# Optimization experiments

Hardware: AMD Instinct MI355X
Metric: run time of the kernel (lower is better)

The kernel has to match this reference:

```python
import jax, jax.numpy as jnp
import numpy as np

KS = 3          # kernel_size
NH = 6          # num_heads
NUM_TOK = KS ** 3  # 27 neighbors per query


def setup_inputs() -> dict:
    key = jax.random.key(0)
    k1, k2, k3 = jax.random.split(key, 3)
    q = jax.random.normal(k1, (1, 40, 40, 40, 96), dtype=jnp.float32)
    k = jax.random.normal(k2, (1, 40, 40, 40, 96), dtype=jnp.float32)
    rpb = jax.random.normal(k3, (NH, KS, KS, KS), dtype=jnp.float32) * 0.02
    return {"q": q, "k": k, "rpb": rpb}


def _offsets():
    # torch.arange(-3//2+1, 3//2+1) == arange(-1, 2); meshgrid 'ij'; stacked -> [27, 3]
    r = jnp.arange(-1, 2, dtype=jnp.float32)
    g = jnp.stack(jnp.meshgrid(r, r, r, indexing="ij"), axis=-1)
    return g.reshape(NUM_TOK, 3)


def reference(q, k, rpb):
    B, H, W, T, C = q.shape
    hd = C // NH
    scale = hd ** -0.5
    N = H * W * T

    # queries: [B, N, nh, hd], pre-scaled
    qh = q.reshape(B, N, NH, hd) * scale

    # zero-pad keys by 1 voxel on each spatial side (matches nnf.pad on channels-first k)
    kp = jnp.pad(jnp.transpose(k, (0, 4, 1, 2, 3)),
                 ((0, 0), (0, 0), (1, 1), (1, 1), (1, 1)))

    # 27 shifted views == torch unfold over a 3x3x3 window (i slowest, matches grid order)
    wins = [kp[:, :, i:i + H, j:j + W, l:l + T]
            for i in range(KS) for j in range(KS) for l in range(KS)]
    Kw = jnp.stack(wins, axis=2)                 # [B, C, 27, H, W, T]
    Kw = Kw.reshape(B, NH, hd, NUM_TOK, N)        # [B, nh, hd, 27, N]

    # attention logits over the 27-token neighborhood
    attn = jnp.einsum("bnhd,bhdkn->bnhk", qh, Kw)  # [B, N, nh, 27]
    attn = attn + rpb.reshape(NH, NUM_TOK)[None, None, :, :]  # relative position bias
    attn = jax.nn.softmax(attn, axis=-1)

    # expected displacement: weighted sum of integer offsets -> [B, N, nh, 3]
    x = jnp.einsum("bnhk,kc->bnhc", attn, _offsets())
    x = x.reshape(B, H, W, T, NH * 3)
    return jnp.transpose(x, (0, 4, 1, 2, 3))      # [B, nh*3, H, W, T]
```

## Files before the change

kernel.cpp:

```cpp
#include <hip/hip_runtime.h>

typedef _Float16 h2 __attribute__((ext_vector_type(2)));

#define DH 40
#define DW 40
#define DT 40
#define NC 96
#define NH 6
#define HD 16
#define NTOK 27
#define NVOX (DH * DW * DT)

#define TX 8
#define TY 4
#define TZ 8
#define HX 10
#define HY 6
#define HZ 10
#define NHALO (HX * HY * HZ)
#define ROW_I4 3

#define TXN (DH / TX)
#define TYN (DW / TY)
#define TZN (DT / TZ)
#define NTILE (TXN * TYN * TZN)
#define NJOB (NTILE * NH)
#define NXCD 8
#define GRID 1504
#define PER_XCD (GRID / NXCD)

__device__ __forceinline__ float dot2acc(h2 a, h2 b, float c) {
    return __builtin_amdgcn_fdot2(a, b, c, false);
}

__device__ __forceinline__ h2 pkrtz(float a, float b) {
    return __builtin_bit_cast(h2, __builtin_amdgcn_cvt_pkrtz(a, b));
}

union I4H {
    int4 v[2];
    h2 h[8];
};

__global__ __launch_bounds__(256) void natt_disp_kernel(
    const float* __restrict__ q,
    const float* __restrict__ k,
    const float* __restrict__ rpb,
    float* __restrict__ out)
{
    __shared__ int4 s_k[NHALO * ROW_I4];

    const int job = (blockIdx.x & (NXCD - 1)) * PER_XCD + (blockIdx.x >> 3);
    if (job >= NJOB) return;

    const int h    = job % NH;
    const int tile = job / NH;
    const int tz = tile % TZN;
    const int ty = (tile / TZN) % TYN;
    const int tx = tile / (TZN * TYN);
    const int x0 = tx * TX, y0 = ty * TY, z0 = tz * TZ;

    const int tid = threadIdx.x;

    float rk[NTOK];
    {
        const float* rb = rpb + h * NTOK;
        #pragma unroll
        for (int kk = 0; kk < NTOK; ++kk) rk[kk] = rb[kk];
    }

    #pragma unroll
    for (int it = 0; it < 3; ++it) {
        const int n = tid + it * 256;
        if (n < NHALO) {
            const int hx = n / (HY * HZ);
            const int r  = n - hx * (HY * HZ);
            const int hy = r / HZ;
            const int hz = r - hy * HZ;
            const int gx = x0 - 1 + hx;
            const int gy = y0 - 1 + hy;
            const int gz = z0 - 1 + hz;
            I4H u;
            u.v[0] = make_int4(0, 0, 0, 0);
            u.v[1] = make_int4(0, 0, 0, 0);
            if (((unsigned)gx < DH) & ((unsigned)gy < DW) & ((unsigned)gz < DT)) {
                const float* src = k + ((size_t)((gx * DW + gy) * DT + gz)) * NC
                                     + h * HD;
                const float4 a = *(const float4*)(src);
                const float4 b = *(const float4*)(src + 4);
                const float4 c = *(const float4*)(src + 8);
                const float4 d = *(const float4*)(src + 12);
                u.h[0] = pkrtz(a.x, a.y);
                u.h[1] = pkrtz(a.z, a.w);
                u.h[2] = pkrtz(b.x, b.y);
                u.h[3] = pkrtz(b.z, b.w);
                u.h[4] = pkrtz(c.x, c.y);
                u.h[5] = pkrtz(c.z, c.w);
                u.h[6] = pkrtz(d.x, d.y);
                u.h[7] = pkrtz(d.z, d.w);
            }
            s_k[n * ROW_I4 + 0] = u.v[0];
            s_k[n * ROW_I4 + 1] = u.v[1];
        }
    }

    const int lz = tid & (TZ - 1);
    const int ly = (tid >> 3) & (TY - 1);
    const int lx = tid >> 5;
    const int vox = ((x0 + lx) * DW + (y0 + ly)) * DT + (z0 + lz);

    h2 qh[8];
    {
        const float4* qv = (const float4*)(q + (size_t)vox * NC + h * HD);
        const float4 a = qv[0], b = qv[1], c = qv[2], d = qv[3];
        qh[0] = pkrtz(a.x, a.y);
        qh[1] = pkrtz(a.z, a.w);
        qh[2] = pkrtz(b.x, b.y);
        qh[3] = pkrtz(b.z, b.w);
        qh[4] = pkrtz(c.x, c.y);
        qh[5] = pkrtz(c.z, c.w);
        qh[6] = pkrtz(d.x, d.y);
        qh[7] = pkrtz(d.z, d.w);
    }

    __syncthreads();

    float l[NTOK];
    #pragma unroll
    for (int i = 0; i < 3; ++i) {
        #pragma unroll
        for (int j = 0; j < 3; ++j) {
            const int base = ((lx + i) * HY + (ly + j)) * HZ + lz;
            #pragma unroll
            for (int ll = 0; ll < 3; ++ll) {
                const int n = base + ll;
                I4H u;
                u.v[0] = s_k[n * ROW_I4 + 0];
                u.v[1] = s_k[n * ROW_I4 + 1];
                float d = 0.0f;
                d = dot2acc(qh[0], u.h[0], d);
                d = dot2acc(qh[1], u.h[1], d);
                d = dot2acc(qh[2], u.h[2], d);
                d = dot2acc(qh[3], u.h[3], d);
                d = dot2acc(qh[4], u.h[4], d);
                d = dot2acc(qh[5], u.h[5], d);
                d = dot2acc(qh[6], u.h[6], d);
                d = dot2acc(qh[7], u.h[7], d);
                const int kk = (i * 3 + j) * 3 + ll;
                l[kk] = fmaf(d, 0.25f, rk[kk]);
            }
        }
    }

    float g0 = fmaxf(fmaxf(l[0],  l[1]),  l[2]);
    float g1 = fmaxf(fmaxf(l[3],  l[4]),  l[5]);
    float g2 = fmaxf(fmaxf(l[6],  l[7]),  l[8]);
    float g3 = fmaxf(fmaxf(l[9],  l[10]), l[11]);
    float g4 = fmaxf(fmaxf(l[12], l[13]), l[14]);
    float g5 = fmaxf(fmaxf(l[15], l[16]), l[17]);
    float g6 = fmaxf(fmaxf(l[18], l[19]), l[20]);
    float g7 = fmaxf(fmaxf(l[21], l[22]), l[23]);
    float g8 = fmaxf(fmaxf(l[24], l[25]), l[26]);
    float t0 = fmaxf(fmaxf(g0, g1), g2);
    float t1 = fmaxf(fmaxf(g3, g4), g5);
    float t2 = fmaxf(fmaxf(g6, g7), g8);
    const float m = fmaxf(fmaxf(t0, t1), t2);

    const float LOG2E = 1.44269504f;
    const float nm2 = -m * LOG2E;
    float e[NTOK];
    #pragma unroll
    for (int kk = 0; kk < NTOK; ++kk)
        e[kk] = exp2f(fmaf(l[kk], LOG2E, nm2));

    float s[9], zp[9];
    #pragma unroll
    for (int g = 0; g < 9; ++g) {
        s[g]  = (e[g * 3] + e[g * 3 + 1]) + e[g * 3 + 2];
        zp[g] = e[g * 3 + 2] - e[g * 3];
    }
    const float sum = ((s[0] + s[1]) + (s[2] + s[3]))
                    + ((s[4] + s[5]) + (s[6] + s[7])) + s[8];
    const float szs = ((zp[0] + zp[1]) + (zp[2] + zp[3]))
                    + ((zp[4] + zp[5]) + (zp[6] + zp[7])) + zp[8];
    const float sxs = ((s[6] + s[7]) + s[8]) - ((s[0] + s[1]) + s[2]);
    const float sys = ((s[2] + s[5]) + s[8]) - ((s[0] + s[3]) + s[6]);

    const float inv = __builtin_amdgcn_rcpf(sum);

    out[((size_t)(h * 3 + 0)) * NVOX + vox] = sxs * inv;
    out[((size_t)(h * 3 + 1)) * NVOX + vox] = sys * inv;
    out[((size_t)(h * 3 + 2)) * NVOX + vox] = szs * inv;
}

extern "C" void kernel_launch(void* const* d_in, const int* in_sizes, int n_in,
                              void* d_out, int out_size, void* d_ws, size_t ws_size,
                              hipStream_t stream) {
    const float* q   = (const float*)d_in[0];
    const float* k   = (const float*)d_in[1];
    const float* rpb = (const float*)d_in[2];
    float* out = (float*)d_out;

    natt_disp_kernel<<<GRID, 256, 0, stream>>>(q, k, rpb, out);
}
```

Measured before the change: 22.11 us.

## Process three jobs per block with register-prefetched K/Q software pipeline

Each block now handles three consecutive (tile, head) jobs instead of one. The global loads of K-halo and Q for the next job are issued into registers before computing the current job, so memory latency overlaps with compute. The grid shrinks to 512 blocks with an XCD-aware mapping, and launch bounds request two blocks per CU. The costs are higher register pressure from the prefetched float4 buffers, extra barriers, and fewer blocks available to hide latency.

```diff
diff --git a/kernel.cpp b/kernel.cpp
--- a/kernel.cpp
+++ b/kernel.cpp
@@ -1,6 +1,6 @@
 #include <hip/hip_runtime.h>
 
-typedef _Float16 h2 __attribute__((ext_vector_type(2)));
+typedef _Float16 hh2 __attribute__((ext_vector_type(2)));
 
 #define DH 40
 #define DW 40
@@ -25,24 +25,23 @@
 #define TZN (DT / TZ)
 #define NTILE (TXN * TYN * TZN)
 #define NJOB (NTILE * NH)
-#define NXCD 8
-#define GRID 1504
-#define PER_XCD (GRID / NXCD)
-
-__device__ __forceinline__ float dot2acc(h2 a, h2 b, float c) {
+#define JPB 3
+#define NBLK (NJOB / JPB)
+#define GRID 512
+
+__device__ __forceinline__ float dot2acc(hh2 a, hh2 b, float c) {
     return __builtin_amdgcn_fdot2(a, b, c, false);
 }
-
-__device__ __forceinline__ h2 pkrtz(float a, float b) {
-    return __builtin_bit_cast(h2, __builtin_amdgcn_cvt_pkrtz(a, b));
+__device__ __forceinline__ hh2 pkrtz(float a, float b) {
+    return __builtin_bit_cast(hh2, __builtin_amdgcn_cvt_pkrtz(a, b));
 }
 
 union I4H {
     int4 v[2];
-    h2 h[8];
+    hh2 h[8];
 };
 
-__global__ __launch_bounds__(256) void natt_disp_kernel(
+__global__ __launch_bounds__(256, 2) void natt_disp_kernel(
     const float* __restrict__ q,
     const float* __restrict__ k,
     const float* __restrict__ rpb,
@@ -50,147 +49,195 @@
 {
     __shared__ int4 s_k[NHALO * ROW_I4];
 
-    const int job = (blockIdx.x & (NXCD - 1)) * PER_XCD + (blockIdx.x >> 3);
-    if (job >= NJOB) return;
-
-    const int h    = job % NH;
-    const int tile = job / NH;
-    const int tz = tile % TZN;
-    const int ty = (tile / TZN) % TYN;
-    const int tx = tile / (TZN * TYN);
-    const int x0 = tx * TX, y0 = ty * TY, z0 = tz * TZ;
+    const int sb = ((blockIdx.x & 7) << 6) | (blockIdx.x >> 3);
+    if (sb >= NBLK) return;
+    const int jbase = sb * JPB;
 
     const int tid = threadIdx.x;
-
-    float rk[NTOK];
-    {
-        const float* rb = rpb + h * NTOK;
-        #pragma unroll
-        for (int kk = 0; kk < NTOK; ++kk) rk[kk] = rb[kk];
-    }
-
-    #pragma unroll
-    for (int it = 0; it < 3; ++it) {
-        const int n = tid + it * 256;
-        if (n < NHALO) {
-            const int hx = n / (HY * HZ);
-            const int r  = n - hx * (HY * HZ);
-            const int hy = r / HZ;
-            const int hz = r - hy * HZ;
-            const int gx = x0 - 1 + hx;
-            const int gy = y0 - 1 + hy;
-            const int gz = z0 - 1 + hz;
-            I4H u;
-            u.v[0] = make_int4(0, 0, 0, 0);
-            u.v[1] = make_int4(0, 0, 0, 0);
-            if (((unsigned)gx < DH) & ((unsigned)gy < DW) & ((unsigned)gz < DT)) {
-                const float* src = k + ((size_t)((gx * DW + gy) * DT + gz)) * NC
-                                     + h * HD;
-                const float4 a = *(const float4*)(src);
-                const float4 b = *(const float4*)(src + 4);
-                const float4 c = *(const float4*)(src + 8);
-                const float4 d = *(const float4*)(src + 12);
-                u.h[0] = pkrtz(a.x, a.y);
-                u.h[1] = pkrtz(a.z, a.w);
-                u.h[2] = pkrtz(b.x, b.y);
-                u.h[3] = pkrtz(b.z, b.w);
-                u.h[4] = pkrtz(c.x, c.y);
-                u.h[5] = pkrtz(c.z, c.w);
-                u.h[6] = pkrtz(d.x, d.y);
-                u.h[7] = pkrtz(d.z, d.w);
-            }
-            s_k[n * ROW_I4 + 0] = u.v[0];
-            s_k[n * ROW_I4 + 1] = u.v[1];
-        }
-    }
-
     const int lz = tid & (TZ - 1);
     const int ly = (tid >> 3) & (TY - 1);
     const int lx = tid >> 5;
-    const int vox = ((x0 + lx) * DW + (y0 + ly)) * DT + (z0 + lz);
-
-    h2 qh[8];
-    {
-        const float4* qv = (const float4*)(q + (size_t)vox * NC + h * HD);
-        const float4 a = qv[0], b = qv[1], c = qv[2], d = qv[3];
-        qh[0] = pkrtz(a.x, a.y);
-        qh[1] = pkrtz(a.z, a.w);
-        qh[2] = pkrtz(b.x, b.y);
-        qh[3] = pkrtz(b.z, b.w);
-        qh[4] = pkrtz(c.x, c.y);
-        qh[5] = pkrtz(c.z, c.w);
-        qh[6] = pkrtz(d.x, d.y);
-        qh[7] = pkrtz(d.z, d.w);
+
+    int voff_[3];
+    int hx_[3], hy_[3], hz_[3];
+    bool has_[3];
+    #pragma unroll
+    for (int s = 0; s < 3; ++s) {
+        const int n = tid + (s << 8);
+        has_[s] = (n < NHALO);
+        const int hx = n / (HY * HZ);
+        const int r  = n - hx * (HY * HZ);
+        const int hy = r / HZ;
+        const int hz = r - hy * HZ;
+        hx_[s] = hx; hy_[s] = hy; hz_[s] = hz;
+        voff_[s] = ((hx * DW + hy) * DT + hz) * NC;
     }
 
-    __syncthreads();
-
-    float l[NTOK];
-    #pragma unroll
-    for (int i = 0; i < 3; ++i) {
-        #pragma unroll
-        for (int j = 0; j < 3; ++j) {
-            const int base = ((lx + i) * HY + (ly + j)) * HZ + lz;
+    auto params = [&](int t, int& hh, int& x0, int& y0, int& z0) {
+        const int job = jbase + t;
+        hh = job % NH;
+        const int tile = job / NH;
+        const int tz = tile % TZN;
+        const int ty = (tile / TZN) % TYN;
+        const int tx = tile / (TZN * TYN);
+        x0 = tx * TX; y0 = ty * TY; z0 = tz * TZ;
+    };
+
+    auto issue = [&](int hh, int x0, int y0, int z0,
+                     float4 (&F)[3][4], bool (&ok)[3], float4 (&Q)[4], int& vox) {
+        const int base0 = (((x0 - 1) * DW + (y0 - 1)) * DT + (z0 - 1)) * NC + hh * HD;
+        #pragma unroll
+        for (int s = 0; s < 3; ++s) {
+            const bool valid = has_[s]
+                & ((unsigned)(x0 - 1 + hx_[s]) < DH)
+                & ((unsigned)(y0 - 1 + hy_[s]) < DW)
+                & ((unsigned)(z0 - 1 + hz_[s]) < DT);
+            ok[s] = valid;
+            const int off = valid ? base0 + voff_[s] : 0;
+            const float* src = k + off;
+            F[s][0] = *(const float4*)(src);
+            F[s][1] = *(const float4*)(src + 4);
+            F[s][2] = *(const float4*)(src + 8);
+            F[s][3] = *(const float4*)(src + 12);
+        }
+        vox = ((x0 + lx) * DW + (y0 + ly)) * DT + (z0 + lz);
+        const float* qs = q + (size_t)vox * NC + hh * HD;
+        Q[0] = *(const float4*)(qs);
+        Q[1] = *(const float4*)(qs + 4);
+        Q[2] = *(const float4*)(qs + 8);
+        Q[3] = *(const float4*)(qs + 12);
+    };
+
+    auto commit = [&](float4 (&F)[3][4], bool (&ok)[3], float4 (&Q)[4], hh2 (&qh)[8]) {
+        #pragma unroll
+        for (int s = 0; s < 3; ++s) {
+            if (has_[s]) {
+                I4H u;
+                u.h[0] = pkrtz(F[s][0].x, F[s][0].y);
+                u.h[1] = pkrtz(F[s][0].z, F[s][0].w);
+                u.h[2] = pkrtz(F[s][1].x, F[s][1].y);
+                u.h[3] = pkrtz(F[s][1].z, F[s][1].w);
+                u.h[4] = pkrtz(F[s][2].x, F[s][2].y);
+                u.h[5] = pkrtz(F[s][2].z, F[s][2].w);
+                u.h[6] = pkrtz(F[s][3].x, F[s][3].y);
+                u.h[7] = pkrtz(F[s][3].z, F[s][3].w);
+                const int4 z4 = make_int4(0, 0, 0, 0);
+                if (!ok[s]) { u.v[0] = z4; u.v[1] = z4; }
+                const int n = tid + (s << 8);
+                s_k[n * ROW_I4 + 0] = u.v[0];
+                s_k[n * ROW_I4 + 1] = u.v[1];
+            }
+        }
+        qh[0] = pkrtz(Q[0].x, Q[0].y);
+        qh[1] = pkrtz(Q[0].z, Q[0].w);
+        qh[2] = pkrtz(Q[1].x, Q[1].y);
+        qh[3] = pkrtz(Q[1].z, Q[1].w);
+        qh[4] = pkrtz(Q[2].x, Q[2].y);
+        qh[5] = pkrtz(Q[2].z, Q[2].w);
+        qh[6] = pkrtz(Q[3].x, Q[3].y);
+        qh[7] = pkrtz(Q[3].z, Q[3].w);
+    };
+
+    auto compute = [&](int hh, hh2 (&qh)[8], int vox) {
+        const float* rb = rpb + hh * NTOK;
+        float rk[NTOK];
+        #pragma unroll
+        for (int kk = 0; kk < NTOK; ++kk) rk[kk] = rb[kk];
+
+        float l[NTOK];
+        #pragma unroll
+        for (int i = 0; i < 3; ++i) {
             #pragma unroll
-            for (int ll = 0; ll < 3; ++ll) {
-                const int n = base + ll;
-                I4H u;
-                u.v[0] = s_k[n * ROW_I4 + 0];
-                u.v[1] = s_k[n * ROW_I4 + 1];
-                float d = 0.0f;
-                d = dot2acc(qh[0], u.h[0], d);
-                d = dot2acc(qh[1], u.h[1], d);
-                d = dot2acc(qh[2], u.h[2], d);
-                d = dot2acc(qh[3], u.h[3], d);
-                d = dot2acc(qh[4], u.h[4], d);
-                d = dot2acc(qh[5], u.h[5], d);
-                d = dot2acc(qh[6], u.h[6], d);
-                d = dot2acc(qh[7], u.h[7], d);
-                const int kk = (i * 3 + j) * 3 + ll;
-                l[kk] = fmaf(d, 0.25f, rk[kk]);
+            for (int j = 0; j < 3; ++j) {
+                const int base = ((lx + i) * HY + (ly + j)) * HZ + lz;
+                #pragma unroll
+                for (int ll = 0; ll < 3; ++ll) {
+                    const int n = base + ll;
+                    I4H u;
+                    u.v[0] = s_k[n * ROW_I4 + 0];
+                    u.v[1] = s_k[n * ROW_I4 + 1];
+                    float d = 0.0f;
+                    d = dot2acc(qh[0], u.h[0], d);
+                    d = dot2acc(qh[1], u.h[1], d);
+                    d = dot2acc(qh[2], u.h[2], d);
+                    d = dot2acc(qh[3], u.h[3], d);
+                    d = dot2acc(qh[4], u.h[4], d);
+                    d = dot2acc(qh[5], u.h[5], d);
+                    d = dot2acc(qh[6], u.h[6], d);
+                    d = dot2acc(qh[7], u.h[7], d);
+                    const int kk = (i * 3 + j) * 3 + ll;
+                    l[kk] = fmaf(d, 0.25f, rk[kk]);
+                }
             }
         }
-    }
-
-    float g0 = fmaxf(fmaxf(l[0],  l[1]),  l[2]);
-    float g1 = fmaxf(fmaxf(l[3],  l[4]),  l[5]);
-    float g2 = fmaxf(fmaxf(l[6],  l[7]),  l[8]);
-    float g3 = fmaxf(fmaxf(l[9],  l[10]), l[11]);
-    float g4 = fmaxf(fmaxf(l[12], l[13]), l[14]);
-    float g5 = fmaxf(fmaxf(l[15], l[16]), l[17]);
-    float g6 = fmaxf(fmaxf(l[18], l[19]), l[20]);
-    float g7 = fmaxf(fmaxf(l[21], l[22]), l[23]);
-    float g8 = fmaxf(fmaxf(l[24], l[25]), l[26]);
-    float t0 = fmaxf(fmaxf(g0, g1), g2);
-    float t1 = fmaxf(fmaxf(g3, g4), g5);
-    float t2 = fmaxf(fmaxf(g6, g7), g8);
-    const float m = fmaxf(fmaxf(t0, t1), t2);
-
-    const float LOG2E = 1.44269504f;
-    const float nm2 = -m * LOG2E;
-    float e[NTOK];
-    #pragma unroll
-    for (int kk = 0; kk < NTOK; ++kk)
-        e[kk] = exp2f(fmaf(l[kk], LOG2E, nm2));
-
-    float s[9], zp[9];
-    #pragma unroll
-    for (int g = 0; g < 9; ++g) {
-        s[g]  = (e[g * 3] + e[g * 3 + 1]) + e[g * 3 + 2];
-        zp[g] = e[g * 3 + 2] - e[g * 3];
-    }
-    const float sum = ((s[0] + s[1]) + (s[2] + s[3]))
-                    + ((s[4] + s[5]) + (s[6] + s[7])) + s[8];
-    const float szs = ((zp[0] + zp[1]) + (zp[2] + zp[3]))
-                    + ((zp[4] + zp[5]) + (zp[6] + zp[7])) + zp[8];
-    const float sxs = ((s[6] + s[7]) + s[8]) - ((s[0] + s[1]) + s[2]);
-    const float sys = ((s[2] + s[5]) + s[8]) - ((s[0] + s[3]) + s[6]);
-
-    const float inv = __builtin_amdgcn_rcpf(sum);
-
-    out[((size_t)(h * 3 + 0)) * NVOX + vox] = sxs * inv;
-    out[((size_t)(h * 3 + 1)) * NVOX + vox] = sys * inv;
-    out[((size_t)(h * 3 + 2)) * NVOX + vox] = szs * inv;
+
+        float g0 = fmaxf(fmaxf(l[0],  l[1]),  l[2]);
+        float g1 = fmaxf(fmaxf(l[3],  l[4]),  l[5]);
+        float g2 = fmaxf(fmaxf(l[6],  l[7]),  l[8]);
+        float g3 = fmaxf(fmaxf(l[9],  l[10]), l[11]);
+        float g4 = fmaxf(fmaxf(l[12], l[13]), l[14]);
+        float g5 = fmaxf(fmaxf(l[15], l[16]), l[17]);
+        float g6 = fmaxf(fmaxf(l[18], l[19]), l[20]);
+        float g7 = fmaxf(fmaxf(l[21], l[22]), l[23]);
+        float g8 = fmaxf(fmaxf(l[24], l[25]), l[26]);
+        float t0 = fmaxf(fmaxf(g0, g1), g2);
+        float t1 = fmaxf(fmaxf(g3, g4), g5);
+        float t2 = fmaxf(fmaxf(g6, g7), g8);
+        const float m = fmaxf(fmaxf(t0, t1), t2);
+
+        const float LOG2E = 1.44269504f;
+        const float nm2 = -m * LOG2E;
+        float e[NTOK];
+        #pragma unroll
+        for (int kk = 0; kk < NTOK; ++kk)
+            e[kk] = exp2f(fmaf(l[kk], LOG2E, nm2));
+
+        float s[9], zp[9];
+        #pragma unroll
+        for (int g = 0; g < 9; ++g) {
+            s[g]  = (e[g * 3] + e[g * 3 + 1]) + e[g * 3 + 2];
+            zp[g] = e[g * 3 + 2] - e[g * 3];
+        }
+        const float sum = ((s[0] + s[1]) + (s[2] + s[3]))
+                        + ((s[4] + s[5]) + (s[6] + s[7])) + s[8];
+        const float szs = ((zp[0] + zp[1]) + (zp[2] + zp[3]))
+                        + ((zp[4] + zp[5]) + (zp[6] + zp[7])) + zp[8];
+        const float sxs = ((s[6] + s[7]) + s[8]) - ((s[0] + s[1]) + s[2]);
+        const float sys = ((s[2] + s[5]) + s[8]) - ((s[0] + s[3]) + s[6]);
+
+        const float inv = __builtin_amdgcn_rcpf(sum);
+
+        out[((size_t)(hh * 3 + 0)) * NVOX + vox] = sxs * inv;
+        out[((size_t)(hh * 3 + 1)) * NVOX + vox] = sys * inv;
+        out[((size_t)(hh * 3 + 2)) * NVOX + vox] = szs * inv;
+    };
+
+    int ha, xa, ya, za; params(0, ha, xa, ya, za);
+    float4 Fa[3][4], Qa[4]; bool oka[3]; int voxa;
+    issue(ha, xa, ya, za, Fa, oka, Qa, voxa);
+    hh2 qha[8];
+    commit(Fa, oka, Qa, qha);
+    __syncthreads();
+
+    int hb, xb, yb, zb; params(1, hb, xb, yb, zb);
+    float4 Fb[3][4], Qb[4]; bool okb[3]; int voxb;
+    issue(hb, xb, yb, zb, Fb, okb, Qb, voxb);
+    compute(ha, qha, voxa);
+    __syncthreads();
+    hh2 qhb[8];
+    commit(Fb, okb, Qb, qhb);
+    __syncthreads();
+
+    int hc, xc, yc, zc; params(2, hc, xc, yc, zc);
+    float4 Fc[3][4], Qc[4]; bool okc[3]; int voxc;
+    issue(hc, xc, yc, zc, Fc, okc, Qc, voxc);
+    compute(hb, qhb, voxb);
+    __syncthreads();
+    hh2 qhc[8];
+    commit(Fc, okc, Qc, qhc);
+    __syncthreads();
+
+    compute(hc, qhc, voxc);
 }
 
 extern "C" void kernel_launch(void* const* d_in, const int* in_sizes, int n_in,
```

After: 25.99 us. 1.18x slower.
